# Kernel tuning notes

Measured on AMD Instinct MI355X. Metric: run time of the kernel, lower is better.

Reference implementation:

```python
import jax, jax.numpy as jnp
import numpy as np

HEADS = 16
EPS = 1e-5

def _ln(x, g, b):
    m = jnp.mean(x, axis=-1, keepdims=True)
    v = jnp.mean((x - m) ** 2, axis=-1, keepdims=True)
    return (x - m) * jax.lax.rsqrt(v + EPS) * g + b

def setup_inputs() -> dict:
    key = jax.random.key(0)
    ks = jax.random.split(key, 12)
    B, N, C, H = 4, 2048, 1024, 4096
    d = {}
    d['x'] = jax.random.normal(ks[0], (B, N, C), jnp.float32)
    d['pos_embed'] = jax.random.normal(ks[1], (1, N, C), jnp.float32)
    # LayerNorm params (normq, normk, normv, norm)
    for nm in ['nq', 'nk', 'nv', 'n']:
        d[nm + '_g'] = jnp.ones((C,), jnp.float32)
        d[nm + '_b'] = jnp.zeros((C,), jnp.float32)
    s = 1.0 / np.sqrt(C)
    d['wq'] = jax.random.uniform(ks[2], (C, C), jnp.float32, -s, s)
    d['bq'] = jnp.zeros((C,), jnp.float32)
    d['wk'] = jax.random.uniform(ks[3], (C, C), jnp.float32, -s, s)
    d['bk'] = jnp.zeros((C,), jnp.float32)
    d['wv'] = jax.random.uniform(ks[4], (C, C), jnp.float32, -s, s)
    d['bv'] = jnp.zeros((C,), jnp.float32)
    d['wp'] = jax.random.uniform(ks[5], (C, C), jnp.float32, -s, s)
    d['bp'] = jnp.zeros((C,), jnp.float32)
    d['w1'] = jax.random.uniform(ks[6], (C, H), jnp.float32, -s, s)
    d['b1'] = jnp.zeros((H,), jnp.float32)
    sh = 1.0 / np.sqrt(H)
    d['w2'] = jax.random.uniform(ks[7], (H, C), jnp.float32, -sh, sh)
    d['b2'] = jnp.zeros((C,), jnp.float32)
    return d

def reference(x, pos_embed, nq_g, nq_b, nk_g, nk_b, nv_g, nv_b, wq, bq, wk, bk, wv, bv, wp, bp, n_g, n_b, w1, b1, w2, b2):
    B, N, C = x.shape
    hd = C // HEADS
    scale = hd ** -0.5
    q_in = x
    k_in = x + pos_embed
    v_in = x + pos_embed
    # Attention (eval mode: dropout = identity)
    q = (_ln(q_in, nq_g, nq_b) @ wq + bq).reshape(B, N, HEADS, hd)
    k = (_ln(k_in, nk_g, nk_b) @ wk + bk).reshape(B, N, HEADS, hd)
    v = (_ln(v_in, nv_g, nv_b) @ wv + bv).reshape(B, N, HEADS, hd)
    attn = jnp.einsum('bqhd,bkhd->bhqk', q, k) * scale
    attn = jax.nn.softmax(attn, axis=-1)
    out = jnp.einsum('bhqk,bkhd->bqhd', attn, v).reshape(B, N, C)
    out = out @ wp + bp
    # residual + MLP
    h = q_in + out
    y = _ln(h, n_g, n_b) @ w1 + b1
    y = jnp.where(y >= 0, y, 0.1 * y)  # LeakyReLU(0.1)
    y = y @ w2 + b2
    return h + y
```

## Files before the change

### kernel.cpp

```cpp
#include <hip/hip_runtime.h>
#include <hip/hip_bf16.h>

#define DEV __device__ __forceinline__

typedef __attribute__((ext_vector_type(8))) short short8;
typedef __attribute__((ext_vector_type(4))) short short4v;
typedef __attribute__((ext_vector_type(4))) float f32x4;
typedef __attribute__((ext_vector_type(2))) int int2v;

constexpr int Bb   = 4;
constexpr int SEQ  = 2048;
constexpr int C    = 1024;
constexpr int HID  = 4096;
constexpr int NH   = 16;
constexpr int HD   = 64;
constexpr int MTOT = Bb * SEQ;

DEV unsigned bfbits(float f) {
  unsigned x = __float_as_uint(f);
  return (x + 0x7fffu + ((x >> 16) & 1u)) >> 16;
}

DEV short f2bf(float f) { return (short)bfbits(f); }

DEV unsigned packrn(float a, float b) {
  unsigned ua = __float_as_uint(a) + 0x8000u;
  unsigned ub = __float_as_uint(b) + 0x8000u;
  return __builtin_amdgcn_perm(ub, ua, 0x07060302u);
}

DEV float fexp2(float x) {
#if __has_builtin(__builtin_amdgcn_exp2f)
  return __builtin_amdgcn_exp2f(x);
#else
  float r;
  asm("v_exp_f32 %0, %1" : "=v"(r) : "v"(x));
  return r;
#endif
}

DEV void gload16(const void* g, void* l) {
  __builtin_amdgcn_global_load_lds((const __attribute__((address_space(1))) void*)g,
                                   (__attribute__((address_space(3))) void*)l, 16, 0, 0);
}

DEV f32x4 mfma16(short4v a, short4v b, f32x4 c) {
#if __has_builtin(__builtin_amdgcn_mfma_f32_16x16x16bf16_1k)
  return __builtin_amdgcn_mfma_f32_16x16x16bf16_1k(a, b, c, 0, 0, 0);
#else
  asm volatile("v_mfma_f32_16x16x16_bf16 %0, %1, %2, %0" : "+v"(c) : "v"(a), "v"(b));
  return c;
#endif
}

DEV void transpose_body(const float* __restrict__ src, short* __restrict__ dst,
                        int R, int Cc) {
  __shared__ float t[32][33];
  int tx = threadIdx.x & 31, ty = threadIdx.x >> 5;
  int c0 = blockIdx.x * 32, r0 = blockIdx.y * 32;
  #pragma unroll
  for (int i = 0; i < 4; i++)
    t[ty + i * 8][tx] = src[(size_t)(r0 + ty + i * 8) * Cc + c0 + tx];
  __syncthreads();
  #pragma unroll
  for (int i = 0; i < 4; i++)
    dst[(size_t)(c0 + ty + i * 8) * R + r0 + tx] = f2bf(t[tx][ty + i * 8]);
}

__global__ void k_transpose_w(const float* __restrict__ src, short* __restrict__ dst,
                              int R, int Cc) {
  transpose_body(src, dst, R, Cc);
}

__global__ void k_transpose_w4(const float* __restrict__ s0, const float* __restrict__ s1,
                               const float* __restrict__ s2, const float* __restrict__ s3,
                               short* __restrict__ d0, short* __restrict__ d1,
                               short* __restrict__ d2, short* __restrict__ d3) {
  const float* s = blockIdx.z == 0 ? s0 : blockIdx.z == 1 ? s1 : blockIdx.z == 2 ? s2 : s3;
  short*       d = blockIdx.z == 0 ? d0 : blockIdx.z == 1 ? d1 : blockIdx.z == 2 ? d2 : d3;
  transpose_body(s, d, C, C);
}

__global__ void k_transpose_v(const short* __restrict__ V, short* __restrict__ Vt) {
  __shared__ short t[32][33];
  int tx = threadIdx.x & 31, ty = threadIdx.x >> 5;
  int plane = blockIdx.z;
  int b = plane >> 4, h = plane & 15;
  int n0 = blockIdx.x * 32, d0 = blockIdx.y * 32;
  #pragma unroll
  for (int i = 0; i < 4; i++)
    t[ty + i * 8][tx] = V[(size_t)(b * SEQ + n0 + ty + i * 8) * C + h * HD + d0 + tx];
  __syncthreads();
  #pragma unroll
  for (int i = 0; i < 4; i++)
    Vt[((size_t)plane * HD + d0 + ty + i * 8) * SEQ + n0 + tx] = t[tx][ty + i * 8];
}

__global__ void k_ln_qkv(const float* __restrict__ x, const float* __restrict__ pos,
                         const float* __restrict__ nqg, const float* __restrict__ nqb,
                         const float* __restrict__ nkg, const float* __restrict__ nkb,
                         const float* __restrict__ nvg, const float* __restrict__ nvb,
                         short* __restrict__ xq, short* __restrict__ xk,
                         short* __restrict__ xv) {
  int row = blockIdx.x, tid = threadIdx.x;
  int n = row & (SEQ - 1);
  float a4[4], p4[4];
  float s1 = 0, s2 = 0, t1 = 0, t2 = 0;
  #pragma unroll
  for (int i = 0; i < 4; i++) {
    int c = tid + i * 256;
    float a = x[(size_t)row * C + c];
    float p = pos[(size_t)n * C + c] + a;
    a4[i] = a; p4[i] = p;
    s1 += a; s2 += a * a; t1 += p; t2 += p * p;
  }
  #pragma unroll
  for (int off = 32; off; off >>= 1) {
    s1 += __shfl_xor(s1, off, 64);
    s2 += __shfl_xor(s2, off, 64);
    t1 += __shfl_xor(t1, off, 64);
    t2 += __shfl_xor(t2, off, 64);
  }
  __shared__ float red[4][4];
  int wave = tid >> 6, lane = tid & 63;
  if (lane == 0) { red[wave][0] = s1; red[wave][1] = s2; red[wave][2] = t1; red[wave][3] = t2; }
  __syncthreads();
  s1 = red[0][0] + red[1][0] + red[2][0] + red[3][0];
  s2 = red[0][1] + red[1][1] + red[2][1] + red[3][1];
  t1 = red[0][2] + red[1][2] + red[2][2] + red[3][2];
  t2 = red[0][3] + red[1][3] + red[2][3] + red[3][3];
  float mq = s1 * (1.f / C), mk = t1 * (1.f / C);
  float rq = rsqrtf(s2 * (1.f / C) - mq * mq + 1e-5f);
  float rk = rsqrtf(t2 * (1.f / C) - mk * mk + 1e-5f);
  #pragma unroll
  for (int i = 0; i < 4; i++) {
    int c = tid + i * 256;
    float nq_ = (a4[i] - mq) * rq;
    float nk_ = (p4[i] - mk) * rk;
    xq[(size_t)row * C + c] = f2bf(nq_ * nqg[c] + nqb[c]);
    xk[(size_t)row * C + c] = f2bf(nk_ * nkg[c] + nkb[c]);
    xv[(size_t)row * C + c] = f2bf(nk_ * nvg[c] + nvb[c]);
  }
}

__global__ void k_ln1(const float* __restrict__ h, const float* __restrict__ g,
                      const float* __restrict__ bta, short* __restrict__ out) {
  int row = blockIdx.x, tid = threadIdx.x;
  float a4[4];
  float s1 = 0, s2 = 0;
  #pragma unroll
  for (int i = 0; i < 4; i++) {
    int c = tid + i * 256;
    float a = h[(size_t)row * C + c];
    a4[i] = a; s1 += a; s2 += a * a;
  }
  #pragma unroll
  for (int off = 32; off; off >>= 1) {
    s1 += __shfl_xor(s1, off, 64);
    s2 += __shfl_xor(s2, off, 64);
  }
  __shared__ float red[4][2];
  int wave = tid >> 6, lane = tid & 63;
  if (lane == 0) { red[wave][0] = s1; red[wave][1] = s2; }
  __syncthreads();
  s1 = red[0][0] + red[1][0] + red[2][0] + red[3][0];
  s2 = red[0][1] + red[1][1] + red[2][1] + red[3][1];
  float m = s1 * (1.f / C);
  float r = rsqrtf(s2 * (1.f / C) - m * m + 1e-5f);
  #pragma unroll
  for (int i = 0; i < 4; i++) {
    int c = tid + i * 256;
    out[(size_t)row * C + c] = f2bf((a4[i] - m) * r * g[c] + bta[c]);
  }
}

template <typename EPI>
DEV void gemm_body(const short* __restrict__ A, const short* __restrict__ Bt,
                   int Kk, short* sA, short* sB, EPI&& epi) {
  const int tid = threadIdx.x;
  const int wave = tid >> 6, lane = tid & 63, quad = lane >> 4, l15 = lane & 15;
  const int wm = (wave >> 1) * 64, wn = (wave & 1) * 64;
  constexpr int BO = 128 * 32;

  const int r0 = tid >> 2, s0 = (tid & 3) * 8;
  const short* gA0 = A + (size_t)r0 * Kk + s0;
  const short* gA1 = A + (size_t)(r0 + 64) * Kk + s0;
  const short* gB0 = Bt + (size_t)r0 * Kk + s0;
  const short* gB1 = Bt + (size_t)(r0 + 64) * Kk + s0;
  short* lA0 = &sA[tid * 8];
  short* lA1 = &sA[(tid + 256) * 8];
  short* lB0 = &sB[tid * 8];
  short* lB1 = &sB[(tid + 256) * 8];

  const f32x4 fzero = {0.f, 0.f, 0.f, 0.f};
  f32x4 acc[4][4];
  #pragma unroll
  for (int mi = 0; mi < 4; mi++)
    #pragma unroll
    for (int ni = 0; ni < 4; ni++) acc[mi][ni] = fzero;

  gload16(gA0, lA0);
  gload16(gA1, lA1);
  gload16(gB0, lB0);
  gload16(gB1, lB1);

  for (int k0 = 0; k0 < Kk; k0 += 32) {
    const int buf = (k0 >> 5) & 1;
    __syncthreads();
    if (k0 + 32 < Kk) {
      const int bo = (buf ^ 1) * BO;
      gload16(gA0 + k0 + 32, lA0 + bo);
      gload16(gA1 + k0 + 32, lA1 + bo);
      gload16(gB0 + k0 + 32, lB0 + bo);
      gload16(gB1 + k0 + 32, lB1 + bo);
    }
    const int bo = buf * BO;
    short8 av[4], bv[4];
    #pragma unroll
    for (int mi = 0; mi < 4; mi++)
      av[mi] = *(const short8*)&sA[bo + (wm + mi * 16 + l15) * 32 + quad * 8];
    #pragma unroll
    for (int ni = 0; ni < 4; ni++)
      bv[ni] = *(const short8*)&sB[bo + (wn + ni * 16 + l15) * 32 + quad * 8];
    #pragma unroll
    for (int mi = 0; mi < 4; mi++)
      #pragma unroll
      for (int ni = 0; ni < 4; ni++)
        acc[mi][ni] = __builtin_amdgcn_mfma_f32_16x16x32_bf16(av[mi], bv[ni], acc[mi][ni], 0, 0, 0);
  }
  epi(acc, wm, wn, quad, l15);
}

template <int MODE>
__global__ __launch_bounds__(256, 2)
void k_gemm(const short* __restrict__ A, const short* __restrict__ Bt,
            const float* __restrict__ bias, const float* __restrict__ resid,
            void* __restrict__ outp, int Nn, int Kk) {
  __shared__ short sA[2 * 128 * 32];
  __shared__ short sB[2 * 128 * 32];
  const int m0 = blockIdx.x * 128, n0 = blockIdx.y * 128;
  gemm_body(A + (size_t)m0 * Kk, Bt + (size_t)n0 * Kk, Kk, sA, sB,
    [&](f32x4 (&acc)[4][4], int wm, int wn, int quad, int l15) {
      float bb[4];
      #pragma unroll
      for (int ni = 0; ni < 4; ni++) bb[ni] = bias[n0 + wn + ni * 16 + l15];
      #pragma unroll
      for (int mi = 0; mi < 4; mi++) {
        #pragma unroll
        for (int ni = 0; ni < 4; ni++) {
          #pragma unroll
          for (int r = 0; r < 4; r++) {
            int row = m0 + wm + mi * 16 + quad * 4 + r;
            int col = n0 + wn + ni * 16 + l15;
            float v = acc[mi][ni][r] + bb[ni];
            if constexpr (MODE == 1) v = v >= 0.f ? v : 0.1f * v;
            if constexpr (MODE == 2)
              ((float*)outp)[(size_t)row * Nn + col] = resid[(size_t)row * Nn + col] + v;
            else
              ((short*)outp)[(size_t)row * Nn + col] = f2bf(v);
          }
        }
      }
    });
}

template <int MODE>
__global__ __launch_bounds__(256, 4)
void k_gemm_n64(const short* __restrict__ A, const short* __restrict__ Bt,
                const float* __restrict__ bias, const float* __restrict__ resid,
                void* __restrict__ outp, int Nn, int Kk) {
  __shared__ short sA[2 * 128 * 32];
  __shared__ short sB[2 * 64 * 32];
  constexpr int BOA = 128 * 32, BOB = 64 * 32;
  const int tid = threadIdx.x;
  const int m0 = blockIdx.x * 128, n0 = blockIdx.y * 64;
  const int wave = tid >> 6, lane = tid & 63, quad = lane >> 4, l15 = lane & 15;
  const int wm = wave * 32;

  const int r0 = tid >> 2, s0 = (tid & 3) * 8;
  const short* gA0 = A + (size_t)(m0 + r0) * Kk + s0;
  const short* gA1 = A + (size_t)(m0 + r0 + 64) * Kk + s0;
  const short* gB0 = Bt + (size_t)(n0 + r0) * Kk + s0;
  short* lA0 = &sA[tid * 8];
  short* lA1 = &sA[(tid + 256) * 8];
  short* lB0 = &sB[tid * 8];

  const f32x4 fzero = {0.f, 0.f, 0.f, 0.f};
  f32x4 acc[2][4];
  #pragma unroll
  for (int mi = 0; mi < 2; mi++)
    #pragma unroll
    for (int ni = 0; ni < 4; ni++) acc[mi][ni] = fzero;

  gload16(gA0, lA0);
  gload16(gA1, lA1);
  gload16(gB0, lB0);

  for (int k0 = 0; k0 < Kk; k0 += 32) {
    const int buf = (k0 >> 5) & 1;
    __syncthreads();
    if (k0 + 32 < Kk) {
      gload16(gA0 + k0 + 32, lA0 + (buf ^ 1) * BOA);
      gload16(gA1 + k0 + 32, lA1 + (buf ^ 1) * BOA);
      gload16(gB0 + k0 + 32, lB0 + (buf ^ 1) * BOB);
    }
    const int boA = buf * BOA, boB = buf * BOB;
    short8 av[2], bv[4];
    #pragma unroll
    for (int mi = 0; mi < 2; mi++)
      av[mi] = *(const short8*)&sA[boA + (wm + mi * 16 + l15) * 32 + quad * 8];
    #pragma unroll
    for (int ni = 0; ni < 4; ni++)
      bv[ni] = *(const short8*)&sB[boB + (ni * 16 + l15) * 32 + quad * 8];
    #pragma unroll
    for (int mi = 0; mi < 2; mi++)
      #pragma unroll
      for (int ni = 0; ni < 4; ni++)
        acc[mi][ni] = __builtin_amdgcn_mfma_f32_16x16x32_bf16(av[mi], bv[ni], acc[mi][ni], 0, 0, 0);
  }

  float bb[4];
  #pragma unroll
  for (int ni = 0; ni < 4; ni++) bb[ni] = bias[n0 + ni * 16 + l15];
  #pragma unroll
  for (int mi = 0; mi < 2; mi++) {
    #pragma unroll
    for (int ni = 0; ni < 4; ni++) {
      #pragma unroll
      for (int r = 0; r < 4; r++) {
        int row = m0 + wm + mi * 16 + quad * 4 + r;
        int col = n0 + ni * 16 + l15;
        float v = acc[mi][ni][r] + bb[ni];
        if constexpr (MODE == 1) v = v >= 0.f ? v : 0.1f * v;
        if constexpr (MODE == 2)
          ((float*)outp)[(size_t)row * Nn + col] = resid[(size_t)row * Nn + col] + v;
        else
          ((short*)outp)[(size_t)row * Nn + col] = f2bf(v);
      }
    }
  }
}

__global__ __launch_bounds__(256, 2)
void k_gemm_qkv(const short* __restrict__ xq, const short* __restrict__ xk,
                const short* __restrict__ xv,
                const short* __restrict__ wqT, const short* __restrict__ wkT,
                const short* __restrict__ wvT,
                const float* __restrict__ bq, const float* __restrict__ bk,
                const float* __restrict__ bv,
                short* __restrict__ Qm, short* __restrict__ Km, short* __restrict__ Vm) {
  __shared__ short sA[2 * 128 * 32];
  __shared__ short sB[2 * 128 * 32];
  const int z = blockIdx.z;
  const short* A    = z == 0 ? xq : z == 1 ? xk : xv;
  const short* Bt   = z == 0 ? wqT : z == 1 ? wkT : wvT;
  const float* bias = z == 0 ? bq : z == 1 ? bk : bv;
  short* outp       = z == 0 ? Qm : z == 1 ? Km : Vm;
  const float scale = z == 0 ? 0.1803368801111244f : 1.0f;
  const int m0 = blockIdx.x * 128, n0 = blockIdx.y * 128;
  gemm_body(A + (size_t)m0 * C, Bt + (size_t)n0 * C, C, sA, sB,
    [&](f32x4 (&acc)[4][4], int wm, int wn, int quad, int l15) {
      float bb[4];
      #pragma unroll
      for (int ni = 0; ni < 4; ni++) bb[ni] = bias[n0 + wn + ni * 16 + l15];
      #pragma unroll
      for (int mi = 0; mi < 4; mi++)
        #pragma unroll
        for (int ni = 0; ni < 4; ni++)
          #pragma unroll
          for (int r = 0; r < 4; r++) {
            int row = m0 + wm + mi * 16 + quad * 4 + r;
            int col = n0 + wn + ni * 16 + l15;
            outp[(size_t)row * C + col] = f2bf((acc[mi][ni][r] + bb[ni]) * scale);
          }
    });
}

__global__ __launch_bounds__(256, 4)
void k_attn(const short* __restrict__ Q, const short* __restrict__ K,
            const short* __restrict__ Vt, short* __restrict__ O) {
  __shared__ __align__(16) short sK[2][64 * 64];
  __shared__ __align__(16) short sV[2][64 * 64];
  const int tid = threadIdx.x;
  const int bh = blockIdx.x;
  const int b = bh >> 4, h = bh & 15;
  const int q0 = blockIdx.y * 128;
  const int wave = tid >> 6, lane = tid & 63, quad = lane >> 4, l15 = lane & 15;
  const int wm = wave * 32;
  const size_t tokBase = (size_t)b * SEQ;

  short8 qf[2][2];
  #pragma unroll
  for (int qi = 0; qi < 2; qi++)
    #pragma unroll
    for (int hf = 0; hf < 2; hf++)
      qf[qi][hf] = *(const short8*)(Q + (tokBase + q0 + wm + qi * 16 + l15) * C
                                    + h * HD + hf * 32 + quad * 8);

  const int r0 = tid >> 3,        c0s = ((tid & 7) ^ (r0 & 7)) * 8;
  const int r1 = (tid + 256) >> 3, c1s = ((tid & 7) ^ (r1 & 7)) * 8;
  const short* gK0 = K + (tokBase + r0) * C + h * HD + c0s;
  const short* gK1 = K + (tokBase + r1) * C + h * HD + c1s;
  const short* gV0 = Vt + ((size_t)bh * HD + r0) * SEQ + c0s;
  const short* gV1 = Vt + ((size_t)bh * HD + r1) * SEQ + c1s;
  short* lK0 = &sK[0][tid * 8];
  short* lK1 = &sK[0][(tid + 256) * 8];
  short* lV0 = &sV[0][tid * 8];
  short* lV1 = &sV[0][(tid + 256) * 8];
  constexpr int BUFO = 64 * 64;

#define STAGE(bufsel, kb) {                                   \
    int kk = (kb) * 64, bo = (bufsel) * BUFO;                 \
    gload16(gK0 + (size_t)kk * C, lK0 + bo);                  \
    gload16(gK1 + (size_t)kk * C, lK1 + bo);                  \
    gload16(gV0 + kk,             lV0 + bo);                  \
    gload16(gV1 + kk,             lV1 + bo); }

  const f32x4 fzero = {0.f, 0.f, 0.f, 0.f};
  const short4v onesv = {0x3F80, 0x3F80, 0x3F80, 0x3F80};
  f32x4 o[2][4];
  f32x4 oSum[2] = {fzero, fzero};
  #pragma unroll
  for (int qi = 0; qi < 2; qi++)
    #pragma unroll
    for (int di = 0; di < 4; di++) o[qi][di] = fzero;

  const int sw = l15 & 7;

  STAGE(0, 0)

  for (int kb = 0; kb < SEQ / 64; kb++) {
    const int buf = kb & 1;
    __syncthreads();
    if (kb + 1 < SEQ / 64) STAGE(buf ^ 1, kb + 1)

    unsigned pk[4][2][2];
    #pragma unroll
    for (int ki = 0; ki < 4; ki++) {
      const int krow = (ki * 16 + l15) * 64;
      short8 a0 = *(const short8*)&sK[buf][krow + ((0 + quad) ^ sw) * 8];
      short8 a1 = *(const short8*)&sK[buf][krow + ((4 + quad) ^ sw) * 8];
      #pragma unroll
      for (int qi = 0; qi < 2; qi++) {
        f32x4 st = __builtin_amdgcn_mfma_f32_16x16x32_bf16(a0, qf[qi][0], fzero, 0, 0, 0);
        st = __builtin_amdgcn_mfma_f32_16x16x32_bf16(a1, qf[qi][1], st, 0, 0, 0);
        float p0 = fexp2(st[0]), p1 = fexp2(st[1]);
        float p2 = fexp2(st[2]), p3 = fexp2(st[3]);
        pk[ki][qi][0] = packrn(p0, p1);
        pk[ki][qi][1] = packrn(p2, p3);
      }
    }

    #pragma unroll
    for (int ki = 0; ki < 4; ki++) {
      short4v bv[4];
      const int g = ((ki * 2 + (quad >> 1)) ^ sw) * 8 + (quad & 1) * 4;
      #pragma unroll
      for (int di = 0; di < 4; di++)
        bv[di] = *(const short4v*)&sV[buf][(di * 16 + l15) * 64 + g];
      #pragma unroll
      for (int qi = 0; qi < 2; qi++) {
        int2v t; t.x = (int)pk[ki][qi][0]; t.y = (int)pk[ki][qi][1];
        short4v aP = __builtin_bit_cast(short4v, t);
        oSum[qi] = mfma16(aP, onesv, oSum[qi]);
        #pragma unroll
        for (int di = 0; di < 4; di++)
          o[qi][di] = mfma16(aP, bv[di], o[qi][di]);
      }
    }
  }
#undef STAGE

  float linv[2][4];
  #pragma unroll
  for (int qi = 0; qi < 2; qi++)
    #pragma unroll
    for (int r = 0; r < 4; r++)
      linv[qi][r] = 1.0f / oSum[qi][r];

  #pragma unroll
  for (int qi = 0; qi < 2; qi++)
    #pragma unroll
    for (int di = 0; di < 4; di++)
      #pragma unroll
      for (int r = 0; r < 4; r++) {
        int row = q0 + wm + qi * 16 + quad * 4 + r;
        int col = h * HD + di * 16 + l15;
        O[(tokBase + row) * C + col] = f2bf(o[qi][di][r] * linv[qi][r]);
      }
}

extern "C" void kernel_launch(void* const* d_in, const int* in_sizes, int n_in,
                              void* d_out, int out_size, void* d_ws, size_t ws_size,
                              hipStream_t stream) {
  const float* x   = (const float*)d_in[0];
  const float* pos = (const float*)d_in[1];
  const float* nqg = (const float*)d_in[2];
  const float* nqb = (const float*)d_in[3];
  const float* nkg = (const float*)d_in[4];
  const float* nkb = (const float*)d_in[5];
  const float* nvg = (const float*)d_in[6];
  const float* nvb = (const float*)d_in[7];
  const float* ng  = (const float*)d_in[8];
  const float* nb  = (const float*)d_in[9];
  const float* wq  = (const float*)d_in[10];
  const float* bq  = (const float*)d_in[11];
  const float* wk  = (const float*)d_in[12];
  const float* bk  = (const float*)d_in[13];
  const float* wv  = (const float*)d_in[14];
  const float* bv  = (const float*)d_in[15];
  const float* wp  = (const float*)d_in[16];
  const float* bp  = (const float*)d_in[17];
  const float* w1  = (const float*)d_in[18];
  const float* b1  = (const float*)d_in[19];
  const float* w2  = (const float*)d_in[20];
  const float* b2  = (const float*)d_in[21];

  char* ws = (char*)d_ws;
  const size_t MB = 1u << 20;
  short* wqT  = (short*)(ws + 0 * MB);
  short* wkT  = (short*)(ws + 2 * MB);
  short* wvT  = (short*)(ws + 4 * MB);
  short* wpT  = (short*)(ws + 6 * MB);
  short* w1T  = (short*)(ws + 8 * MB);
  short* w2T  = (short*)(ws + 16 * MB);
  short* xq   = (short*)(ws + 24 * MB);
  short* xk   = (short*)(ws + 40 * MB);
  short* xv   = (short*)(ws + 56 * MB);
  short* Qm   = (short*)(ws + 72 * MB);
  short* Km   = (short*)(ws + 88 * MB);
  short* Vm   = (short*)(ws + 104 * MB);
  short* Vt   = (short*)(ws + 120 * MB);
  short* y1   = (short*)(ws + 72 * MB);
  short* Ob   = xk;
  short* hln  = xq;
  float* hbuf = (float*)(ws + 136 * MB);
  (void)ws_size; (void)in_sizes; (void)n_in; (void)out_size;

  dim3 blk(256);
  k_transpose_w4<<<dim3(32, 32, 4), blk, 0, stream>>>(wq, wk, wv, wp, wqT, wkT, wvT, wpT);
  k_transpose_w<<<dim3(128, 32), blk, 0, stream>>>(w1, w1T, C, HID);
  k_transpose_w<<<dim3(32, 128), blk, 0, stream>>>(w2, w2T, HID, C);
  k_ln_qkv<<<dim3(MTOT), blk, 0, stream>>>(x, pos, nqg, nqb, nkg, nkb, nvg, nvb, xq, xk, xv);
  k_gemm_qkv<<<dim3(MTOT / 128, C / 128, 3), blk, 0, stream>>>(xq, xk, xv, wqT, wkT, wvT,
                                                               bq, bk, bv, Qm, Km, Vm);
  k_transpose_v<<<dim3(SEQ / 32, HD / 32, Bb * NH), blk, 0, stream>>>(Vm, Vt);
  k_attn<<<dim3(Bb * NH, SEQ / 128), blk, 0, stream>>>(Qm, Km, Vt, Ob);
  k_gemm<2><<<dim3(MTOT / 128, C / 128), blk, 0, stream>>>(Ob, wpT, bp, x, hbuf, C, C);
  k_ln1<<<dim3(MTOT), blk, 0, stream>>>(hbuf, ng, nb, hln);
  k_gemm<1><<<dim3(MTOT / 128, HID / 128), blk, 0, stream>>>(hln, w1T, b1, nullptr, y1, HID, C);
  k_gemm<2><<<dim3(MTOT / 128, C / 128), blk, 0, stream>>>(y1, w2T, b2, hbuf, (float*)d_out, C, HID);
}
```

Measured before the change: 547.9 us.

## Use triple-buffered GEMM with vmcnt-based waits for the final MLP projection

Replaces the unused n64 GEMM variant with a 128x128-tile GEMM that keeps three LDS stages in flight. It waits on the vector-memory counter instead of a full __syncthreads, so global loads for two stages ahead overlap with MFMA work. This kernel is used only for the K=4096 second MLP GEMM. The extra stage raises LDS use to 48KB per block, which may limit occupancy, and the raw s_waitcnt asm relies on assumptions about how the compiler orders loads.

```diff
diff --git a/kernel.cpp b/kernel.cpp
--- a/kernel.cpp
+++ b/kernel.cpp
@@ -265,71 +265,82 @@
 }
 
 template <int MODE>
-__global__ __launch_bounds__(256, 4)
-void k_gemm_n64(const short* __restrict__ A, const short* __restrict__ Bt,
-                const float* __restrict__ bias, const float* __restrict__ resid,
-                void* __restrict__ outp, int Nn, int Kk) {
-  __shared__ short sA[2 * 128 * 32];
-  __shared__ short sB[2 * 64 * 32];
-  constexpr int BOA = 128 * 32, BOB = 64 * 32;
+__global__ __launch_bounds__(256, 2)
+void k_gemm_p3(const short* __restrict__ A, const short* __restrict__ Bt,
+               const float* __restrict__ bias, const float* __restrict__ resid,
+               void* __restrict__ outp, int Nn, int Kk) {
+  __shared__ short sA[3 * 128 * 32];
+  __shared__ short sB[3 * 128 * 32];
+  constexpr int BO = 128 * 32;
   const int tid = threadIdx.x;
-  const int m0 = blockIdx.x * 128, n0 = blockIdx.y * 64;
   const int wave = tid >> 6, lane = tid & 63, quad = lane >> 4, l15 = lane & 15;
-  const int wm = wave * 32;
+  const int wm = (wave >> 1) * 64, wn = (wave & 1) * 64;
+  const int m0 = blockIdx.x * 128, n0 = blockIdx.y * 128;
+  const short* Ab = A + (size_t)m0 * Kk;
+  const short* Bb_ = Bt + (size_t)n0 * Kk;
 
   const int r0 = tid >> 2, s0 = (tid & 3) * 8;
-  const short* gA0 = A + (size_t)(m0 + r0) * Kk + s0;
-  const short* gA1 = A + (size_t)(m0 + r0 + 64) * Kk + s0;
-  const short* gB0 = Bt + (size_t)(n0 + r0) * Kk + s0;
+  const short* gA0 = Ab + (size_t)r0 * Kk + s0;
+  const short* gA1 = Ab + (size_t)(r0 + 64) * Kk + s0;
+  const short* gB0 = Bb_ + (size_t)r0 * Kk + s0;
+  const short* gB1 = Bb_ + (size_t)(r0 + 64) * Kk + s0;
   short* lA0 = &sA[tid * 8];
   short* lA1 = &sA[(tid + 256) * 8];
   short* lB0 = &sB[tid * 8];
+  short* lB1 = &sB[(tid + 256) * 8];
 
   const f32x4 fzero = {0.f, 0.f, 0.f, 0.f};
-  f32x4 acc[2][4];
-  #pragma unroll
-  for (int mi = 0; mi < 2; mi++)
+  f32x4 acc[4][4];
+  #pragma unroll
+  for (int mi = 0; mi < 4; mi++)
     #pragma unroll
     for (int ni = 0; ni < 4; ni++) acc[mi][ni] = fzero;
 
-  gload16(gA0, lA0);
-  gload16(gA1, lA1);
-  gload16(gB0, lB0);
-
-  for (int k0 = 0; k0 < Kk; k0 += 32) {
-    const int buf = (k0 >> 5) & 1;
-    __syncthreads();
-    if (k0 + 32 < Kk) {
-      gload16(gA0 + k0 + 32, lA0 + (buf ^ 1) * BOA);
-      gload16(gA1 + k0 + 32, lA1 + (buf ^ 1) * BOA);
-      gload16(gB0 + k0 + 32, lB0 + (buf ^ 1) * BOB);
-    }
-    const int boA = buf * BOA, boB = buf * BOB;
-    short8 av[2], bv[4];
-    #pragma unroll
-    for (int mi = 0; mi < 2; mi++)
-      av[mi] = *(const short8*)&sA[boA + (wm + mi * 16 + l15) * 32 + quad * 8];
+  const int nk = Kk >> 5;
+
+#define STG(j) {                                        \
+    const int bo_ = ((j) % 3) * BO;                     \
+    const int kk_ = (j) << 5;                           \
+    gload16(gA0 + kk_, lA0 + bo_);                      \
+    gload16(gA1 + kk_, lA1 + bo_);                      \
+    gload16(gB0 + kk_, lB0 + bo_);                      \
+    gload16(gB1 + kk_, lB1 + bo_); }
+
+  STG(0)
+  if (nk > 1) STG(1)
+
+  for (int k = 0; k < nk; k++) {
+    if (k + 1 < nk) asm volatile("s_waitcnt vmcnt(4)" ::: "memory");
+    else            asm volatile("s_waitcnt vmcnt(0)" ::: "memory");
+    __builtin_amdgcn_s_barrier();
+    if (k + 2 < nk) STG(k + 2)
+    const int bo = (k % 3) * BO;
+    short8 av[4], bv[4];
+    #pragma unroll
+    for (int mi = 0; mi < 4; mi++)
+      av[mi] = *(const short8*)&sA[bo + (wm + mi * 16 + l15) * 32 + quad * 8];
     #pragma unroll
     for (int ni = 0; ni < 4; ni++)
-      bv[ni] = *(const short8*)&sB[boB + (ni * 16 + l15) * 32 + quad * 8];
-    #pragma unroll
-    for (int mi = 0; mi < 2; mi++)
+      bv[ni] = *(const short8*)&sB[bo + (wn + ni * 16 + l15) * 32 + quad * 8];
+    #pragma unroll
+    for (int mi = 0; mi < 4; mi++)
       #pragma unroll
       for (int ni = 0; ni < 4; ni++)
         acc[mi][ni] = __builtin_amdgcn_mfma_f32_16x16x32_bf16(av[mi], bv[ni], acc[mi][ni], 0, 0, 0);
   }
+#undef STG
 
   float bb[4];
   #pragma unroll
-  for (int ni = 0; ni < 4; ni++) bb[ni] = bias[n0 + ni * 16 + l15];
-  #pragma unroll
-  for (int mi = 0; mi < 2; mi++) {
+  for (int ni = 0; ni < 4; ni++) bb[ni] = bias[n0 + wn + ni * 16 + l15];
+  #pragma unroll
+  for (int mi = 0; mi < 4; mi++) {
     #pragma unroll
     for (int ni = 0; ni < 4; ni++) {
       #pragma unroll
       for (int r = 0; r < 4; r++) {
         int row = m0 + wm + mi * 16 + quad * 4 + r;
-        int col = n0 + ni * 16 + l15;
+        int col = n0 + wn + ni * 16 + l15;
         float v = acc[mi][ni][r] + bb[ni];
         if constexpr (MODE == 1) v = v >= 0.f ? v : 0.1f * v;
         if constexpr (MODE == 2)
@@ -549,5 +560,5 @@
   k_gemm<2><<<dim3(MTOT / 128, C / 128), blk, 0, stream>>>(Ob, wpT, bp, x, hbuf, C, C);
   k_ln1<<<dim3(MTOT), blk, 0, stream>>>(hbuf, ng, nb, hln);
   k_gemm<1><<<dim3(MTOT / 128, HID / 128), blk, 0, stream>>>(hln, w1T, b1, nullptr, y1, HID, C);
-  k_gemm<2><<<dim3(MTOT / 128, C / 128), blk, 0, stream>>>(y1, w2T, b2, hbuf, (float*)d_out, C, HID);
-}
+  k_gemm_p3<2><<<dim3(MTOT / 128, C / 128), blk, 0, stream>>>(y1, w2T, b2, hbuf, (float*)d_out, C, HID);
+}
```

New measurement: 538.0 us. About the same (-1.8%).
